# Kernel optimization log

Hardware: AMD Instinct MI355X
Metric: run time of the kernel (lower is better)

## Reference

```python
import jax, jax.numpy as jnp
import numpy as np

B, D, H, E = 32768, 128, 512, 16

def setup_inputs() -> dict:
    key = jax.random.key(0)
    ks = jax.random.split(key, 5)
    x = jax.random.normal(ks[0], (B, 1, D), dtype=jnp.float32)
    s1 = 1.0 / float(np.sqrt(H))   # init_ uses last-dim size: w1 last dim = H
    s2 = 1.0 / float(np.sqrt(D))   # w2 last dim = D
    sg = 1.0 / float(np.sqrt(D))   # nn.Linear(D, E) default init scale
    w1 = jax.random.uniform(ks[1], (E, D, H), minval=-s1, maxval=s1, dtype=jnp.float32)
    w2 = jax.random.uniform(ks[2], (E, H, D), minval=-s2, maxval=s2, dtype=jnp.float32)
    wg = jax.random.uniform(ks[3], (D, E), minval=-sg, maxval=sg, dtype=jnp.float32)
    bg = jax.random.uniform(ks[4], (E,), minval=-sg, maxval=sg, dtype=jnp.float32)
    return {"x": x, "w1": w1, "w2": w2, "wg": wg, "bg": bg}

def reference(x, w1, w2, wg, bg):
    xt = x[:, 0, :]                                   # (B, D); seq dim is 1 by construction
    logits = xt @ wg + bg                             # (B, E)
    topk_vals, topk_idx = jax.lax.top_k(logits, 1)    # (B, 1) each
    scores = jax.nn.softmax(topk_vals, axis=-1)       # (B, 1); all ones for k=1
    # every expert processes every token (faithful to the reference)
    hidden = jax.nn.gelu(jnp.einsum('bd,edh->ebh', xt, w1), approximate=False)  # (E, B, H)
    eout = jnp.einsum('ebh,ehd->ebd', hidden, w2)     # (E, B, D)
    # gather selected expert per token, scale, sum over k
    sel = jnp.take_along_axis(eout.transpose(1, 0, 2), topk_idx[:, :, None], axis=1)  # (B, 1, D)
    return (sel * scores[:, :, None]).sum(axis=1)     # (B, D)
```

## Files before the change

kernel.cpp:

```cpp
#include <hip/hip_runtime.h>
#include <hip/hip_bf16.h>
#include <math.h>

#define NB 32768
#define DD 128
#define HH 512
#define EE 16

typedef __attribute__((ext_vector_type(8))) short short8;
typedef __attribute__((ext_vector_type(4))) float f32x4;

__device__ __forceinline__ unsigned int pk_bf16(float a, float b) {
  float2 t; t.x = a; t.y = b;
  __hip_bfloat162 h = __float22bfloat162_rn(t);
  union { __hip_bfloat162 h; unsigned int u; } cv; cv.h = h;
  return cv.u;
}

__device__ __forceinline__ float gelu_f(float v) {
  float z = v * 0.70710678118654752f;
  float a = fabsf(z);
  float t = 1.0f / (1.0f + 0.3275911f * a);
  float y = t * (0.254829592f + t * (-0.284496736f + t * (1.421413741f +
            t * (-1.453152027f + t * 1.061405429f))));
  float r = 1.0f - y * __expf(-a * a);
  r = z < 0.0f ? -r : r;
  return 0.5f * v * (1.0f + r);
}

__global__ __launch_bounds__(256, 3) void prep_kernel(
    const float* __restrict__ x, const float* __restrict__ w1,
    const float* __restrict__ w2, const float* __restrict__ wg,
    const float* __restrict__ bg,
    unsigned short* __restrict__ w1T, unsigned short* __restrict__ w2T,
    int* __restrict__ counts, int* __restrict__ rows) {
  __shared__ __align__(16) char smem[34816];

  int tid = threadIdx.x;
  int bid = blockIdx.x;

  if (bid < 512) {
    float (*sx)[132] = (float(*)[132])smem;
    int* lslot = (int*)(smem + 33792);
    int* lexp  = (int*)(smem + 34048);
    int* lcnt  = (int*)(smem + 34304);
    int* gbase = (int*)(smem + 34368);

    int base = bid * 64;
    if (tid < EE) lcnt[tid] = 0;
    {
      int r = tid >> 2, c0 = (tid & 3) * 32;
      const f32x4* src = (const f32x4*)(x + (size_t)(base + r) * DD + c0);
      #pragma unroll
      for (int i = 0; i < 8; ++i)
        *(f32x4*)&sx[r][c0 + i * 4] = src[i];
    }

    int wv = tid >> 6, l = tid & 63;
    int ep = l & 7;
    int ds = l >> 3;

    double wr0[16], wr1[16];
    {
      const float* wp = wg + (ds * 16) * EE + 2 * ep;
      #pragma unroll
      for (int i = 0; i < 16; ++i) {
        float2 w2v = *(const float2*)(wp + i * EE);
        wr0[i] = (double)w2v.x; wr1[i] = (double)w2v.y;
      }
    }
    double bg0 = (double)bg[2 * ep], bg1 = (double)bg[2 * ep + 1];
    __syncthreads();

    for (int rr = 0; rr < 16; ++rr) {
      int row = wv * 16 + rr;
      double a0 = 0.0, a1 = 0.0;
      #pragma unroll
      for (int i = 0; i < 4; ++i) {
        f32x4 xv = *(const f32x4*)&sx[row][ds * 16 + i * 4];
        #pragma unroll
        for (int c = 0; c < 4; ++c) {
          double xd = (double)xv[c];
          a0 += xd * wr0[i * 4 + c];
          a1 += xd * wr1[i * 4 + c];
        }
      }
      #pragma unroll
      for (int off = 8; off < 64; off <<= 1) {
        a0 += __shfl_xor(a0, off);
        a1 += __shfl_xor(a1, off);
      }
      a0 += bg0; a1 += bg1;
      double bv = a0; int be = 2 * ep;
      if (a1 > a0) { bv = a1; be = 2 * ep + 1; }
      #pragma unroll
      for (int off = 1; off < 8; off <<= 1) {
        double ov = __shfl_xor(bv, off);
        int oe = __shfl_xor(be, off);
        if (ov > bv || (ov == bv && oe < be)) { bv = ov; be = oe; }
      }
      if (l == 0) {
        lslot[row] = atomicAdd(&lcnt[be], 1);
        lexp[row] = be;
      }
    }
    __syncthreads();
    if (tid < EE && lcnt[tid] > 0)
      gbase[tid] = atomicAdd(&counts[tid * 16], lcnt[tid]);
    __syncthreads();
    if (tid < 64) {
      int e2 = lexp[tid];
      rows[e2 * NB + gbase[e2] + lslot[tid]] = base + tid;
    }
  } else {
    float* sT = (float*)smem;
    int tb = bid - 512;
    const float* src; unsigned short* dst; int sstride, dstride;
    if (tb < 256) {
      int e2 = tb >> 4, t = tb & 15;
      int d0 = (t >> 3) * 64, h0 = (t & 7) * 64;
      src = w1 + ((size_t)e2 * DD + d0) * HH + h0; sstride = HH;
      dst = w1T + (size_t)e2 * HH * DD + (size_t)h0 * DD + d0; dstride = DD;
    } else {
      int t2 = tb - 256;
      int e2 = t2 >> 4, t = t2 & 15;
      int h0 = (t >> 1) * 64, d0 = (t & 1) * 64;
      src = w2 + ((size_t)e2 * HH + h0) * DD + d0; sstride = DD;
      dst = w2T + (size_t)e2 * DD * HH + (size_t)d0 * HH + h0; dstride = HH;
    }
    int rr = tid >> 4, c4 = tid & 15;
    #pragma unroll
    for (int j = 0; j < 4; ++j) {
      int sr = rr + 16 * j;
      f32x4 v = *(const f32x4*)(src + (size_t)sr * sstride + c4 * 4);
      #pragma unroll
      for (int i = 0; i < 4; ++i) sT[sr * 65 + c4 * 4 + i] = v[i];
    }
    __syncthreads();
    #pragma unroll
    for (int j = 0; j < 4; ++j) {
      int R = rr + 16 * j;
      float f0 = sT[(4 * c4 + 0) * 65 + R];
      float f1 = sT[(4 * c4 + 1) * 65 + R];
      float f2 = sT[(4 * c4 + 2) * 65 + R];
      float f3 = sT[(4 * c4 + 3) * 65 + R];
      uint2 pkd; pkd.x = pk_bf16(f0, f1); pkd.y = pk_bf16(f2, f3);
      *(uint2*)(dst + (size_t)R * dstride + 4 * c4) = pkd;
    }
  }
}

__global__ __launch_bounds__(256, 3) void moe_gemm(
    const float* __restrict__ x, const unsigned short* __restrict__ w1T,
    const unsigned short* __restrict__ w2T, const int* __restrict__ counts,
    const int* __restrict__ rows, float* __restrict__ out) {
  int e = blockIdx.y;
  int cnt = counts[e * 16];
  int base = blockIdx.x * 64;
  if (base >= cnt) return;

  __shared__ unsigned short sW1[64][136];
  __shared__ unsigned short sW2[DD][72];
  __shared__ unsigned short sH[4][16][72];

  int tid = threadIdx.x;
  int wv = tid >> 6, l = tid & 63;
  int lm = l & 15, q = l >> 4;

  int i0 = base + wv * 16 + lm;
  int ci0 = i0 < cnt ? i0 : cnt - 1;
  int grow = rows[e * NB + ci0];

  short8 xf[4];
  {
    const float* xr = x + (size_t)grow * DD;
    #pragma unroll
    for (int ks = 0; ks < 4; ++ks) {
      const f32x4* p = (const f32x4*)(xr + ks * 32 + q * 8);
      f32x4 v0 = p[0], v1 = p[1];
      union { short8 s; unsigned int u[4]; } pk;
      pk.u[0] = pk_bf16(v0[0], v0[1]);
      pk.u[1] = pk_bf16(v0[2], v0[3]);
      pk.u[2] = pk_bf16(v1[0], v1[1]);
      pk.u[3] = pk_bf16(v1[2], v1[3]);
      xf[ks] = pk.s;
    }
  }

  f32x4 acc[8];
  #pragma unroll
  for (int dt = 0; dt < 8; ++dt) acc[dt] = (f32x4){0.f, 0.f, 0.f, 0.f};

  const unsigned short* w1e = w1T + (size_t)e * HH * DD;
  const unsigned short* w2e = w2T + (size_t)e * DD * HH;

  for (int hc = 0; hc < 8; ++hc) {
    int h0 = hc * 64;
    {
      const uint4* src = (const uint4*)(w1e + (size_t)h0 * DD);
      #pragma unroll
      for (int i = 0; i < 4; ++i) {
        int u = tid + i * 256;
        int r = u >> 4, c = u & 15;
        *(uint4*)&sW1[r][c * 8] = src[u];
      }
    }
    {
      #pragma unroll
      for (int i = 0; i < 4; ++i) {
        int u = tid + i * 256;
        int r = u >> 3, c = u & 7;
        const uint4* src = (const uint4*)(w2e + (size_t)r * HH + h0);
        *(uint4*)&sW2[r][c * 8] = src[c];
      }
    }
    __syncthreads();

    #pragma unroll
    for (int ht = 0; ht < 4; ++ht) {
      f32x4 ha = (f32x4){0.f, 0.f, 0.f, 0.f};
      #pragma unroll
      for (int ks = 0; ks < 4; ++ks) {
        short8 a = *(const short8*)&sW1[ht * 16 + lm][ks * 32 + q * 8];
        ha = __builtin_amdgcn_mfma_f32_16x16x32_bf16(a, xf[ks], ha, 0, 0, 0);
      }
      uint2 wa;
      wa.x = pk_bf16(gelu_f(ha[0]), gelu_f(ha[1]));
      wa.y = pk_bf16(gelu_f(ha[2]), gelu_f(ha[3]));
      *(uint2*)&sH[wv][lm][ht * 16 + q * 4] = wa;
    }

    #pragma unroll
    for (int ks = 0; ks < 2; ++ks) {
      short8 b0 = *(const short8*)&sH[wv][lm][ks * 32 + q * 8];
      #pragma unroll
      for (int dt = 0; dt < 8; ++dt) {
        short8 a = *(const short8*)&sW2[dt * 16 + lm][ks * 32 + q * 8];
        acc[dt] = __builtin_amdgcn_mfma_f32_16x16x32_bf16(a, b0, acc[dt], 0, 0, 0);
      }
    }
    __syncthreads();
  }

  if (i0 < cnt) {
    float* op = out + (size_t)grow * DD + q * 4;
    #pragma unroll
    for (int dt = 0; dt < 8; ++dt)
      *(f32x4*)(op + dt * 16) = acc[dt];
  }
}

extern "C" void kernel_launch(void* const* d_in, const int* in_sizes, int n_in,
                              void* d_out, int out_size, void* d_ws, size_t ws_size,
                              hipStream_t stream) {
  const float* x  = (const float*)d_in[0];
  const float* w1 = (const float*)d_in[1];
  const float* w2 = (const float*)d_in[2];
  const float* wg = (const float*)d_in[3];
  const float* bg = (const float*)d_in[4];
  float* out = (float*)d_out;

  int* counts = (int*)d_ws;
  int* rows   = (int*)((char*)d_ws + 1024);
  unsigned short* w1T = (unsigned short*)((char*)d_ws + 1024 + (size_t)EE * NB * 4);
  unsigned short* w2T = w1T + (size_t)EE * HH * DD;

  hipMemsetAsync(d_ws, 0, 1024, stream);
  hipLaunchKernelGGL(prep_kernel, dim3(1024), dim3(256), 0, stream,
                     x, w1, w2, wg, bg, w1T, w2T, counts, rows);
  hipLaunchKernelGGL(moe_gemm, dim3(NB / 64, EE), dim3(256), 0, stream,
                     x, w1T, w2T, counts, rows, out);
}
```

Measured before the change: 144.2 us.

## Prefetch next weight chunk into registers, cheapen GELU erf, pair gating rows

```diff
diff --git a/kernel.cpp b/kernel.cpp
--- a/kernel.cpp
+++ b/kernel.cpp
@@ -20,9 +20,8 @@
 __device__ __forceinline__ float gelu_f(float v) {
   float z = v * 0.70710678118654752f;
   float a = fabsf(z);
-  float t = 1.0f / (1.0f + 0.3275911f * a);
-  float y = t * (0.254829592f + t * (-0.284496736f + t * (1.421413741f +
-            t * (-1.453152027f + t * 1.061405429f))));
+  float t = 1.0f / (1.0f + 0.47047f * a);
+  float y = t * (0.3480242f + t * (-0.0958798f + t * 0.7478556f));
   float r = 1.0f - y * __expf(-a * a);
   r = z < 0.0f ? -r : r;
   return 0.5f * v * (1.0f + r);
@@ -72,36 +71,42 @@
     double bg0 = (double)bg[2 * ep], bg1 = (double)bg[2 * ep + 1];
     __syncthreads();
 
-    for (int rr = 0; rr < 16; ++rr) {
-      int row = wv * 16 + rr;
-      double a0 = 0.0, a1 = 0.0;
+    for (int rr = 0; rr < 16; rr += 2) {
+      int rowA = wv * 16 + rr, rowB = rowA + 1;
+      double a0 = 0.0, a1 = 0.0, c0 = 0.0, c1 = 0.0;
       #pragma unroll
       for (int i = 0; i < 4; ++i) {
-        f32x4 xv = *(const f32x4*)&sx[row][ds * 16 + i * 4];
+        f32x4 xa = *(const f32x4*)&sx[rowA][ds * 16 + i * 4];
+        f32x4 xb = *(const f32x4*)&sx[rowB][ds * 16 + i * 4];
         #pragma unroll
         for (int c = 0; c < 4; ++c) {
-          double xd = (double)xv[c];
-          a0 += xd * wr0[i * 4 + c];
-          a1 += xd * wr1[i * 4 + c];
+          double xda = (double)xa[c], xdb = (double)xb[c];
+          a0 += xda * wr0[i * 4 + c];
+          a1 += xda * wr1[i * 4 + c];
+          c0 += xdb * wr0[i * 4 + c];
+          c1 += xdb * wr1[i * 4 + c];
         }
       }
       #pragma unroll
       for (int off = 8; off < 64; off <<= 1) {
-        a0 += __shfl_xor(a0, off);
-        a1 += __shfl_xor(a1, off);
-      }
-      a0 += bg0; a1 += bg1;
-      double bv = a0; int be = 2 * ep;
-      if (a1 > a0) { bv = a1; be = 2 * ep + 1; }
+        a0 += __shfl_xor(a0, off); a1 += __shfl_xor(a1, off);
+        c0 += __shfl_xor(c0, off); c1 += __shfl_xor(c1, off);
+      }
+      a0 += bg0; a1 += bg1; c0 += bg0; c1 += bg1;
+      double bvA = a0; int beA = 2 * ep;
+      if (a1 > a0) { bvA = a1; beA = 2 * ep + 1; }
+      double bvB = c0; int beB = 2 * ep;
+      if (c1 > c0) { bvB = c1; beB = 2 * ep + 1; }
       #pragma unroll
       for (int off = 1; off < 8; off <<= 1) {
-        double ov = __shfl_xor(bv, off);
-        int oe = __shfl_xor(be, off);
-        if (ov > bv || (ov == bv && oe < be)) { bv = ov; be = oe; }
+        double ovA = __shfl_xor(bvA, off); int oeA = __shfl_xor(beA, off);
+        double ovB = __shfl_xor(bvB, off); int oeB = __shfl_xor(beB, off);
+        if (ovA > bvA || (ovA == bvA && oeA < beA)) { bvA = ovA; beA = oeA; }
+        if (ovB > bvB || (ovB == bvB && oeB < beB)) { bvB = ovB; beB = oeB; }
       }
       if (l == 0) {
-        lslot[row] = atomicAdd(&lcnt[be], 1);
-        lexp[row] = be;
+        lslot[rowA] = atomicAdd(&lcnt[beA], 1); lexp[rowA] = beA;
+        lslot[rowB] = atomicAdd(&lcnt[beB], 1); lexp[rowB] = beB;
       }
     }
     __syncthreads();
@@ -171,6 +176,31 @@
   int ci0 = i0 < cnt ? i0 : cnt - 1;
   int grow = rows[e * NB + ci0];
 
+  const unsigned short* w1e = w1T + (size_t)e * HH * DD;
+  const unsigned short* w2e = w2T + (size_t)e * DD * HH;
+
+  int u2r = tid >> 3, u2c = tid & 7;
+  uint4 p1[4], p2[4];
+  auto load_chunk = [&](int hc) {
+    int h0 = hc * 64;
+    const uint4* s1 = (const uint4*)(w1e + (size_t)h0 * DD);
+    #pragma unroll
+    for (int i = 0; i < 4; ++i) p1[i] = s1[tid + i * 256];
+    #pragma unroll
+    for (int i = 0; i < 4; ++i)
+      p2[i] = ((const uint4*)(w2e + (size_t)(u2r + i * 32) * HH + h0))[u2c];
+  };
+  auto write_chunk = [&]() {
+    #pragma unroll
+    for (int i = 0; i < 4; ++i) {
+      int u = tid + i * 256;
+      *(uint4*)&sW1[u >> 4][(u & 15) * 8] = p1[i];
+    }
+    #pragma unroll
+    for (int i = 0; i < 4; ++i)
+      *(uint4*)&sW2[u2r + i * 32][u2c * 8] = p2[i];
+  };
+
   short8 xf[4];
   {
     const float* xr = x + (size_t)grow * DD;
@@ -191,30 +221,12 @@
   #pragma unroll
   for (int dt = 0; dt < 8; ++dt) acc[dt] = (f32x4){0.f, 0.f, 0.f, 0.f};
 
-  const unsigned short* w1e = w1T + (size_t)e * HH * DD;
-  const unsigned short* w2e = w2T + (size_t)e * DD * HH;
+  load_chunk(0);
+  write_chunk();
+  __syncthreads();
 
   for (int hc = 0; hc < 8; ++hc) {
-    int h0 = hc * 64;
-    {
-      const uint4* src = (const uint4*)(w1e + (size_t)h0 * DD);
-      #pragma unroll
-      for (int i = 0; i < 4; ++i) {
-        int u = tid + i * 256;
-        int r = u >> 4, c = u & 15;
-        *(uint4*)&sW1[r][c * 8] = src[u];
-      }
-    }
-    {
-      #pragma unroll
-      for (int i = 0; i < 4; ++i) {
-        int u = tid + i * 256;
-        int r = u >> 3, c = u & 7;
-        const uint4* src = (const uint4*)(w2e + (size_t)r * HH + h0);
-        *(uint4*)&sW2[r][c * 8] = src[c];
-      }
-    }
-    __syncthreads();
+    if (hc < 7) load_chunk(hc + 1);
 
     #pragma unroll
     for (int ht = 0; ht < 4; ++ht) {
@@ -240,6 +252,10 @@
       }
     }
     __syncthreads();
+    if (hc < 7) {
+      write_chunk();
+      __syncthreads();
+    }
   }
 
   if (i0 < cnt) {
```

Result: slower. 166.0 us (+15.2%).
